# Optimization experiments

Hardware: AMD Instinct MI355X
Metric: run time of the kernel (lower is better)

## Reference

```python
import jax, jax.numpy as jnp
import numpy as np

N_EMBD = 768
N_HEAD = 8
HEAD_DIM = N_EMBD // N_HEAD
EPS = 1e-5


def _layernorm(x, g, b):
    mu = jnp.mean(x, axis=-1, keepdims=True)
    var = jnp.mean(jnp.square(x - mu), axis=-1, keepdims=True)
    return (x - mu) * jax.lax.rsqrt(var + EPS) * g + b


def _new_gelu(x):
    c = jnp.sqrt(2.0 / jnp.pi).astype(x.dtype)
    return 0.5 * x * (1.0 + jnp.tanh(c * (x + 0.044715 * x * x * x)))


def setup_inputs() -> dict:
    key = jax.random.key(0)
    ks = jax.random.split(key, 10)
    B, T, C = 16, 1024, N_EMBD
    s = lambda fan_in: 1.0 / np.sqrt(fan_in)
    inp = {
        "x": jax.random.normal(ks[0], (B, T, C), dtype=jnp.float32),
        "ln1_g": jnp.ones((C,), jnp.float32),
        "ln1_b": jnp.zeros((C,), jnp.float32),
        "attn_w": jax.random.normal(ks[1], (C, 3 * C), jnp.float32) * s(C),
        "attn_b": jnp.zeros((3 * C,), jnp.float32),
        "proj_w": jax.random.normal(ks[2], (C, C), jnp.float32) * s(C),
        "proj_b": jnp.zeros((C,), jnp.float32),
        "ln2_g": jnp.ones((C,), jnp.float32),
        "ln2_b": jnp.zeros((C,), jnp.float32),
        "fc_w": jax.random.normal(ks[3], (C, 4 * C), jnp.float32) * s(C),
        "fc_b": jnp.zeros((4 * C,), jnp.float32),
        "fc2_w": jax.random.normal(ks[4], (4 * C, C), jnp.float32) * s(4 * C),
        "fc2_b": jnp.zeros((C,), jnp.float32),
    }
    return inp


def reference(x, ln1_g, ln1_b, attn_w, attn_b, proj_w, proj_b,
              ln2_g, ln2_b, fc_w, fc_b, fc2_w, fc2_b):
    B, T, C = x.shape
    H, D = N_HEAD, HEAD_DIM
    scale = 1.0 / np.sqrt(D)

    # --- attention branch ---
    h = _layernorm(x, ln1_g, ln1_b)
    qkv = h @ attn_w + attn_b                       # [B,T,3C]
    q, k, v = jnp.split(qkv, 3, axis=-1)
    q = q.reshape(B, T, H, D).transpose(0, 2, 1, 3)  # [B,H,T,D]
    k = k.reshape(B, T, H, D).transpose(0, 2, 1, 3)
    v = v.reshape(B, T, H, D).transpose(0, 2, 1, 3)
    att = jnp.einsum("bhqd,bhkd->bhqk", q, k) * scale
    causal = jnp.tril(jnp.ones((T, T), bool))
    att = jnp.where(causal, att, -jnp.inf)
    att = jax.nn.softmax(att, axis=-1)
    y = jnp.einsum("bhqk,bhkd->bhqd", att, v)        # [B,H,T,D]
    y = y.transpose(0, 2, 1, 3).reshape(B, T, C)
    y = y @ proj_w + proj_b
    x = x + y

    # --- MLP branch ---
    h2 = _layernorm(x, ln2_g, ln2_b)
    h2 = _new_gelu(h2 @ fc_w + fc_b)
    x = x + (h2 @ fc2_w + fc2_b)
    return x
```

## Files before the change

kernel.cpp:

```cpp
#include <hip/hip_runtime.h>


typedef __bf16 bf16;
typedef __bf16 bf16x8 __attribute__((ext_vector_type(8)));
typedef __bf16 bf16x4 __attribute__((ext_vector_type(4)));
typedef __bf16 bf16x2 __attribute__((ext_vector_type(2)));
typedef float f32x4 __attribute__((ext_vector_type(4)));

__device__ __forceinline__ void async_copy16(const void* g, void* l)
{
    __builtin_amdgcn_global_load_lds((__attribute__((address_space(1))) void*)g,
                                     (__attribute__((address_space(3))) void*)l,
                                     16, 0, 0);
}

__device__ __forceinline__ void bar_nodrain()
{
    __builtin_amdgcn_sched_barrier(0);
    __asm__ volatile("" ::: "memory");
    __builtin_amdgcn_s_barrier();
    __asm__ volatile("" ::: "memory");
    __builtin_amdgcn_sched_barrier(0);
}

__global__ __launch_bounds__(256) void wtrans4(const float* __restrict__ aw, bf16* __restrict__ awT,
                                               const float* __restrict__ pw, bf16* __restrict__ pwT,
                                               const float* __restrict__ fw, bf16* __restrict__ fwT,
                                               const float* __restrict__ f2w, bf16* __restrict__ f2wT)
{
    __shared__ float tile[32][33];
    int id = blockIdx.x;
    const float* in; bf16* out; int R, C, nx;
    if (id < 1728)      { in = aw;  out = awT;  R = 768;  C = 2304; nx = 72; }
    else if (id < 2304) { in = pw;  out = pwT;  R = 768;  C = 768;  nx = 24; id -= 1728; }
    else if (id < 4608) { in = fw;  out = fwT;  R = 768;  C = 3072; nx = 96; id -= 2304; }
    else                { in = f2w; out = f2wT; R = 3072; C = 768;  nx = 24; id -= 4608; }
    const int c0 = (id % nx) * 32, r0 = (id / nx) * 32;
    const int tx = threadIdx.x, ty = threadIdx.y;
#pragma unroll
    for (int i = 0; i < 4; ++i)
        tile[ty + i * 8][tx] = in[(size_t)(r0 + ty + i * 8) * C + c0 + tx];
    __syncthreads();
#pragma unroll
    for (int i = 0; i < 4; ++i)
        out[(size_t)(c0 + ty + i * 8) * R + r0 + tx] = (bf16)tile[tx][ty + i * 8];
}

template <typename TIN>
__global__ __launch_bounds__(256) void ln_kernel(const TIN* __restrict__ x,
                                                 const float* __restrict__ g,
                                                 const float* __restrict__ bb,
                                                 bf16* __restrict__ out)
{
    const int wave = threadIdx.x >> 6, lane = threadIdx.x & 63;
    const size_t row = (size_t)blockIdx.x * 4 + wave;
    const TIN* xr = x + row * 768;
    float v[12];
    float s = 0.f;
#pragma unroll
    for (int c = 0; c < 3; ++c) {
        if constexpr (sizeof(TIN) == 2) {
            const bf16x4 t4 = *(const bf16x4*)(xr + c * 256 + lane * 4);
#pragma unroll
            for (int j = 0; j < 4; ++j) { v[c * 4 + j] = (float)t4[j]; s += v[c * 4 + j]; }
        } else {
            const float4 t4 = *(const float4*)(xr + c * 256 + lane * 4);
            v[c * 4 + 0] = t4.x; v[c * 4 + 1] = t4.y;
            v[c * 4 + 2] = t4.z; v[c * 4 + 3] = t4.w;
            s += t4.x + t4.y + t4.z + t4.w;
        }
    }
#pragma unroll
    for (int off = 32; off >= 1; off >>= 1) s += __shfl_xor(s, off, 64);
    const float mu = s * (1.f / 768.f);
    float q = 0.f;
#pragma unroll
    for (int i = 0; i < 12; ++i) { const float d = v[i] - mu; q += d * d; }
#pragma unroll
    for (int off = 32; off >= 1; off >>= 1) q += __shfl_xor(q, off, 64);
    const float rs = rsqrtf(q * (1.f / 768.f) + 1e-5f);
#pragma unroll
    for (int c = 0; c < 3; ++c) {
        const float4 gv = *(const float4*)(g + c * 256 + lane * 4);
        const float4 bv = *(const float4*)(bb + c * 256 + lane * 4);
        bf16x4 ov;
        ov[0] = (bf16)((v[c * 4 + 0] - mu) * rs * gv.x + bv.x);
        ov[1] = (bf16)((v[c * 4 + 1] - mu) * rs * gv.y + bv.y);
        ov[2] = (bf16)((v[c * 4 + 2] - mu) * rs * gv.z + bv.z);
        ov[3] = (bf16)((v[c * 4 + 3] - mu) * rs * gv.w + bv.w);
        *(bf16x4*)(out + row * 768 + c * 256 + lane * 4) = ov;
    }
}

template <int EPI, int TN>
__global__ __launch_bounds__(256) void gemm_bt(const bf16* __restrict__ A,
                                               const bf16* __restrict__ Bt,
                                               const float* __restrict__ bias,
                                               const void* __restrict__ res,
                                               void* __restrict__ out,
                                               const int M, const int N, const int K)
{
    constexpr int NT_W = TN / 32;
    constexpr int NCPB = (TN * 8) / 256;
    __shared__ bf16 sA[2 * 128 * 32];
    __shared__ bf16 sB[2 * TN * 32];
    const int t = threadIdx.x;
    const int wave = t >> 6, lane = t & 63;
    const int quad = lane >> 4, l16 = lane & 15;
    const int bm0 = blockIdx.x * 128, bn0 = blockIdx.y * TN;
    const int wm = (wave >> 1) * 64, wn = (wave & 1) * (TN / 2);

    const f32x4 z4 = {0.f, 0.f, 0.f, 0.f};
    f32x4 acc[4][NT_W];
#pragma unroll
    for (int i = 0; i < 4; ++i)
#pragma unroll
        for (int j = 0; j < NT_W; ++j) acc[i][j] = z4;

    const bf16* gAp[4]; bf16* lAp[4];
#pragma unroll
    for (int c = 0; c < 4; ++c) {
        const int j = c * 256 + t;
        const int img = j >> 9, r = (j >> 2) & 127, k8 = j & 3;
        gAp[c] = A + (size_t)(bm0 + r) * K + img * 32 + k8 * 8;
        lAp[c] = sA + j * 8;
    }
    const bf16* gBp[NCPB]; bf16* lBp[NCPB];
#pragma unroll
    for (int c = 0; c < NCPB; ++c) {
        const int j = c * 256 + t;
        const int img = j / (TN * 4), r = (j % (TN * 4)) >> 2, k8 = j & 3;
        gBp[c] = Bt + (size_t)(bn0 + r) * K + img * 32 + k8 * 8;
        lBp[c] = sB + j * 8;
    }

    for (int kt = 0; kt < K; kt += 64) {
        __syncthreads();
#pragma unroll
        for (int c = 0; c < 4; ++c) async_copy16(gAp[c] + kt, lAp[c]);
#pragma unroll
        for (int c = 0; c < NCPB; ++c) async_copy16(gBp[c] + kt, lBp[c]);
        __syncthreads();

#pragma unroll
        for (int ks = 0; ks < 2; ++ks) {
            bf16x8 af[4], bfm[NT_W];
#pragma unroll
            for (int mt = 0; mt < 4; ++mt)
                af[mt] = *(const bf16x8*)(sA + ks * 4096 +
                                          (wm + mt * 16 + l16) * 32 + quad * 8);
#pragma unroll
            for (int nt = 0; nt < NT_W; ++nt)
                bfm[nt] = *(const bf16x8*)(sB + ks * (TN * 32) +
                                           (wn + nt * 16 + l16) * 32 + quad * 8);
#pragma unroll
            for (int mt = 0; mt < 4; ++mt)
#pragma unroll
                for (int nt = 0; nt < NT_W; ++nt)
                    acc[mt][nt] = __builtin_amdgcn_mfma_f32_16x16x32_bf16(
                        af[mt], bfm[nt], acc[mt][nt], 0, 0, 0);
        }
    }

    const int rb = bm0 + wm + quad * 4;
    const int cb = bn0 + wn + l16;
#pragma unroll
    for (int mt = 0; mt < 4; ++mt) {
#pragma unroll
        for (int nt = 0; nt < NT_W; ++nt) {
            const int col = cb + nt * 16;
            const float bv = bias[col];
#pragma unroll
            for (int reg = 0; reg < 4; ++reg) {
                const size_t idx = (size_t)(rb + mt * 16 + reg) * N + col;
                float v = acc[mt][nt][reg] + bv;
                if constexpr (EPI == 1) {
                    ((bf16*)out)[idx] = (bf16)(v + ((const float*)res)[idx]);
                } else if constexpr (EPI == 2) {
                    const float u = v;
                    const float a2 = 1.5957691216057308f *
                                     (u + 0.044715f * u * u * u);
                    v = u / (1.f + __expf(-a2));
                    ((bf16*)out)[idx] = (bf16)v;
                } else if constexpr (EPI == 3) {
                    ((float*)out)[idx] = v + (float)((const bf16*)res)[idx];
                } else {
                    ((bf16*)out)[idx] = (bf16)v;
                }
            }
        }
    }
}

__global__ __launch_bounds__(256) void attn_kernel(const bf16* __restrict__ qkv,
                                                   bf16* __restrict__ aout)
{
    constexpr int T = 1024, C3 = 2304, HD = 96, CC = 768;
    __shared__ bf16 sK[64 * 104];
    __shared__ bf16 sV[96 * 72];
    __shared__ bf16 sP[4][16 * 76];
    const int tid = threadIdx.x;
    const int wave = tid >> 6, lane = tid & 63;
    const int quad = lane >> 4, l16 = lane & 15;
    const int bh = blockIdx.x, b = bh >> 3, h = bh & 7;
    const float scale = 0.10206207261596575f;

    const int qAi = blockIdx.y;
    const int qBi = 15 - qAi;
    const int q0A = qAi * 64 + wave * 16;
    const int q0B = qBi * 64 + wave * 16;

    const bf16* kgbase = qkv + (size_t)b * T * C3 + CC + h * HD;
    const bf16* vgbase = qkv + (size_t)b * T * C3 + 2 * CC + h * HD;
    bf16* sPw = &sP[wave][0];

    int kKey[3], kCh[3], vKey2[3], vDq[3];
#pragma unroll
    for (int c = 0; c < 3; ++c) {
        const int j = c * 256 + tid;
        kKey[c] = j / 12; kCh[c] = j - kKey[c] * 12;
        vKey2[c] = (j & 31) * 2; vDq[c] = j >> 5;
    }

    const bf16* qrA = qkv + (size_t)(b * T + q0A + l16) * C3 + h * HD + quad * 8;
    const bf16* qrB = qkv + (size_t)(b * T + q0B + l16) * C3 + h * HD + quad * 8;
    const bf16x8 aQA0 = *(const bf16x8*)(qrA);
    const bf16x8 aQA1 = *(const bf16x8*)(qrA + 32);
    const bf16x8 aQA2 = *(const bf16x8*)(qrA + 64);
    const bf16x8 aQB0 = *(const bf16x8*)(qrB);
    const bf16x8 aQB1 = *(const bf16x8*)(qrB + 32);
    const bf16x8 aQB2 = *(const bf16x8*)(qrB + 64);

    const f32x4 z4 = {0.f, 0.f, 0.f, 0.f};
    f32x4 oA[6], oB[6];
#pragma unroll
    for (int i = 0; i < 6; ++i) { oA[i] = z4; oB[i] = z4; }
    float lA[4] = {0.f, 0.f, 0.f, 0.f}, lB[4] = {0.f, 0.f, 0.f, 0.f};

    bf16x8 kreg[3];
    bf16x4 va[3], vb[3];
    auto issue_tile = [&](const int kk0) {
#pragma unroll
        for (int c = 0; c < 3; ++c) {
            kreg[c] = *(const bf16x8*)(kgbase + (size_t)(kk0 + kKey[c]) * C3 +
                                       kCh[c] * 8);
            const bf16* p0 = vgbase + (size_t)(kk0 + vKey2[c]) * C3 + vDq[c] * 4;
            va[c] = *(const bf16x4*)p0;
            vb[c] = *(const bf16x4*)(p0 + C3);
        }
    };

    auto process = [&](const bf16x8& Q0, const bf16x8& Q1, const bf16x8& Q2,
                       f32x4 (&o)[6], float (&lrow)[4],
                       const int q0, const int kk0, const bool diag) {
        f32x4 s[4];
#pragma unroll
        for (int i = 0; i < 4; ++i) s[i] = z4;
#pragma unroll
        for (int nt = 0; nt < 4; ++nt) {
            const bf16* kp = sK + (nt * 16 + l16) * 104 + quad * 8;
            const bf16x8 b0 = *(const bf16x8*)(kp);
            const bf16x8 b1 = *(const bf16x8*)(kp + 32);
            const bf16x8 b2 = *(const bf16x8*)(kp + 64);
            s[nt] = __builtin_amdgcn_mfma_f32_16x16x32_bf16(Q0, b0, s[nt], 0, 0, 0);
            s[nt] = __builtin_amdgcn_mfma_f32_16x16x32_bf16(Q1, b1, s[nt], 0, 0, 0);
            s[nt] = __builtin_amdgcn_mfma_f32_16x16x32_bf16(Q2, b2, s[nt], 0, 0, 0);
        }

        float psum[4] = {0.f, 0.f, 0.f, 0.f};
#pragma unroll
        for (int nt = 0; nt < 4; ++nt)
#pragma unroll
            for (int reg = 0; reg < 4; ++reg) {
                float v = s[nt][reg] * scale;
                if (diag) {
                    const int qr = q0 + quad * 4 + reg;
                    const int key = kk0 + nt * 16 + l16;
                    v = (key > qr) ? -1e30f : v;
                }
                const float p = __expf(fminf(v, 30.f));
                s[nt][reg] = p;
                psum[reg] += p;
            }

#pragma unroll
        for (int nt = 0; nt < 4; ++nt)
#pragma unroll
            for (int reg = 0; reg < 4; ++reg)
                sPw[(quad * 4 + reg) * 76 + nt * 16 + l16] = (bf16)s[nt][reg];
        __asm__ volatile("s_waitcnt lgkmcnt(0)" ::: "memory");

#pragma unroll
        for (int off = 1; off < 16; off <<= 1)
#pragma unroll
            for (int reg = 0; reg < 4; ++reg)
                psum[reg] += __shfl_xor(psum[reg], off, 64);
#pragma unroll
        for (int reg = 0; reg < 4; ++reg) lrow[reg] += psum[reg];

        const bf16x8 aP0 = *(const bf16x8*)(sPw + l16 * 76 + quad * 8);
        const bf16x8 aP1 = *(const bf16x8*)(sPw + l16 * 76 + 32 + quad * 8);
#pragma unroll
        for (int dd = 0; dd < 6; ++dd) {
            const bf16* vp = sV + (dd * 16 + l16) * 72 + quad * 8;
            const bf16x8 v0 = *(const bf16x8*)(vp);
            const bf16x8 v1 = *(const bf16x8*)(vp + 32);
            o[dd] = __builtin_amdgcn_mfma_f32_16x16x32_bf16(aP0, v0, o[dd], 0, 0, 0);
            o[dd] = __builtin_amdgcn_mfma_f32_16x16x32_bf16(aP1, v1, o[dd], 0, 0, 0);
        }
    };

    issue_tile(0);

    for (int kb = 0; kb <= qBi; ++kb) {
        const int kk0 = kb * 64;

        bar_nodrain();

#pragma unroll
        for (int c = 0; c < 3; ++c)
            *(bf16x8*)(sK + kKey[c] * 104 + kCh[c] * 8) = kreg[c];
#pragma unroll
        for (int c = 0; c < 3; ++c) {
#pragma unroll
            for (int jj = 0; jj < 4; ++jj) {
                bf16x2 pk; pk[0] = va[c][jj]; pk[1] = vb[c][jj];
                *(bf16x2*)(sV + (vDq[c] * 4 + jj) * 72 + vKey2[c]) = pk;
            }
        }

        if (kb < qBi) issue_tile(kk0 + 64);

        __asm__ volatile("s_waitcnt lgkmcnt(0)" ::: "memory");
        bar_nodrain();

        process(aQB0, aQB1, aQB2, oB, lB, q0B, kk0, kb == qBi);
        if (kb <= qAi)
            process(aQA0, aQA1, aQA2, oA, lA, q0A, kk0, kb == qAi);
    }

    bf16* opA = aout + (size_t)(b * T + q0A + quad * 4) * CC + h * HD + l16;
    bf16* opB = aout + (size_t)(b * T + q0B + quad * 4) * CC + h * HD + l16;
#pragma unroll
    for (int reg = 0; reg < 4; ++reg) {
        const float invA = 1.f / lA[reg];
        const float invB = 1.f / lB[reg];
#pragma unroll
        for (int dd = 0; dd < 6; ++dd) {
            opA[(size_t)reg * CC + dd * 16] = (bf16)(oA[dd][reg] * invA);
            opB[(size_t)reg * CC + dd * 16] = (bf16)(oB[dd][reg] * invB);
        }
    }
}

extern "C" void kernel_launch(void* const* d_in, const int* in_sizes, int n_in,
                              void* d_out, int out_size, void* d_ws, size_t ws_size,
                              hipStream_t stream)
{
    const float* x      = (const float*)d_in[0];
    const float* ln1_g  = (const float*)d_in[1];
    const float* ln1_b  = (const float*)d_in[2];
    const float* attn_w = (const float*)d_in[3];
    const float* attn_b = (const float*)d_in[4];
    const float* proj_w = (const float*)d_in[5];
    const float* proj_b = (const float*)d_in[6];
    const float* ln2_g  = (const float*)d_in[7];
    const float* ln2_b  = (const float*)d_in[8];
    const float* fc_w   = (const float*)d_in[9];
    const float* fc_b   = (const float*)d_in[10];
    const float* fc2_w  = (const float*)d_in[11];
    const float* fc2_b  = (const float*)d_in[12];

    char* ws = (char*)d_ws;
    bf16*  attn_wT = (bf16*)(ws + 0);
    bf16*  proj_wT = (bf16*)(ws + 3538944);
    bf16*  fc_wT   = (bf16*)(ws + 4718592);
    bf16*  fc2_wT  = (bf16*)(ws + 9437184);
    bf16*  hbuf    = (bf16*)(ws + 14155776);
    bf16*  qkv     = (bf16*)(ws + 39321600);
    bf16*  x1      = (bf16*)(ws + 39321600);
    bf16*  act     = (bf16*)(ws + 64487424);

    wtrans4<<<6912, dim3(32, 8), 0, stream>>>(attn_w, attn_wT, proj_w, proj_wT,
                                              fc_w, fc_wT, fc2_w, fc2_wT);

    ln_kernel<float><<<4096, 256, 0, stream>>>(x, ln1_g, ln1_b, hbuf);

    gemm_bt<0, 128><<<dim3(128, 18), 256, 0, stream>>>(
        hbuf, attn_wT, attn_b, nullptr, qkv, 16384, 2304, 768);

    attn_kernel<<<dim3(128, 8), 256, 0, stream>>>(qkv, hbuf);

    gemm_bt<1, 128><<<dim3(128, 6), 256, 0, stream>>>(
        hbuf, proj_wT, proj_b, x, x1, 16384, 768, 768);

    ln_kernel<bf16><<<4096, 256, 0, stream>>>(x1, ln2_g, ln2_b, hbuf);

    for (int c = 0; c < 2; ++c) {
        const size_t ro = (size_t)c * 8192;
        gemm_bt<2, 128><<<dim3(64, 24), 256, 0, stream>>>(
            hbuf + ro * 768, fc_wT, fc_b, nullptr, act, 8192, 3072, 768);
        gemm_bt<3, 64><<<dim3(64, 12), 256, 0, stream>>>(
            act, fc2_wT, fc2_b, x1 + ro * 768,
            (float*)d_out + ro * 768, 8192, 768, 3072);
    }
}
```

Baseline: 595.3 us.

## Double-buffer GEMM LDS tiles to overlap async loads with MFMA

The GEMM main loop used to load a 64-wide K slab into LDS and then compute on it, with a full barrier on each side. It now uses two 32-wide K buffers: the next slab is prefetched with async global-to-LDS copies while MFMAs run on the current one, followed by a vmcnt wait and a lightweight barrier. This aims to hide global memory latency behind compute. The cost is twice as many loop iterations and barriers for the same K range, since each step now covers only 32 of K.

New measurement: 609.7 us. 1.02x slower.

```diff
diff --git a/kernel.cpp b/kernel.cpp
--- a/kernel.cpp
+++ b/kernel.cpp
@@ -101,9 +101,10 @@
                                                const int M, const int N, const int K)
 {
     constexpr int NT_W = TN / 32;
-    constexpr int NCPB = (TN * 8) / 256;
-    __shared__ bf16 sA[2 * 128 * 32];
-    __shared__ bf16 sB[2 * TN * 32];
+    constexpr int NCPA = 2;
+    constexpr int NCPB = (TN * 4) / 256;
+    __shared__ bf16 sA[2][128 * 32];
+    __shared__ bf16 sB[2][TN * 32];
     const int t = threadIdx.x;
     const int wave = t >> 6, lane = t & 63;
     const int quad = lane >> 4, l16 = lane & 15;
@@ -117,49 +118,54 @@
 #pragma unroll
         for (int j = 0; j < NT_W; ++j) acc[i][j] = z4;
 
-    const bf16* gAp[4]; bf16* lAp[4];
-#pragma unroll
-    for (int c = 0; c < 4; ++c) {
+    const bf16* gAp[NCPA]; int lAo[NCPA];
+#pragma unroll
+    for (int c = 0; c < NCPA; ++c) {
         const int j = c * 256 + t;
-        const int img = j >> 9, r = (j >> 2) & 127, k8 = j & 3;
-        gAp[c] = A + (size_t)(bm0 + r) * K + img * 32 + k8 * 8;
-        lAp[c] = sA + j * 8;
-    }
-    const bf16* gBp[NCPB]; bf16* lBp[NCPB];
+        const int r = j >> 2, k8 = j & 3;
+        gAp[c] = A + (size_t)(bm0 + r) * K + k8 * 8;
+        lAo[c] = j * 8;
+    }
+    const bf16* gBp[NCPB]; int lBo[NCPB];
 #pragma unroll
     for (int c = 0; c < NCPB; ++c) {
         const int j = c * 256 + t;
-        const int img = j / (TN * 4), r = (j % (TN * 4)) >> 2, k8 = j & 3;
-        gBp[c] = Bt + (size_t)(bn0 + r) * K + img * 32 + k8 * 8;
-        lBp[c] = sB + j * 8;
-    }
-
-    for (int kt = 0; kt < K; kt += 64) {
-        __syncthreads();
-#pragma unroll
-        for (int c = 0; c < 4; ++c) async_copy16(gAp[c] + kt, lAp[c]);
-#pragma unroll
-        for (int c = 0; c < NCPB; ++c) async_copy16(gBp[c] + kt, lBp[c]);
-        __syncthreads();
-
-#pragma unroll
-        for (int ks = 0; ks < 2; ++ks) {
-            bf16x8 af[4], bfm[NT_W];
-#pragma unroll
-            for (int mt = 0; mt < 4; ++mt)
-                af[mt] = *(const bf16x8*)(sA + ks * 4096 +
-                                          (wm + mt * 16 + l16) * 32 + quad * 8);
+        const int r = j >> 2, k8 = j & 3;
+        gBp[c] = Bt + (size_t)(bn0 + r) * K + k8 * 8;
+        lBo[c] = j * 8;
+    }
+
+    auto stage = [&](const int buf, const int kt) {
+#pragma unroll
+        for (int c = 0; c < NCPA; ++c) async_copy16(gAp[c] + kt, &sA[buf][lAo[c]]);
+#pragma unroll
+        for (int c = 0; c < NCPB; ++c) async_copy16(gBp[c] + kt, &sB[buf][lBo[c]]);
+    };
+
+    stage(0, 0);
+    __syncthreads();
+
+    int cur = 0;
+    for (int kt = 0; kt < K; kt += 32) {
+        if (kt + 32 < K) stage(cur ^ 1, kt + 32);
+
+        bf16x8 af[4], bfm[NT_W];
+#pragma unroll
+        for (int mt = 0; mt < 4; ++mt)
+            af[mt] = *(const bf16x8*)(&sA[cur][(wm + mt * 16 + l16) * 32 + quad * 8]);
+#pragma unroll
+        for (int nt = 0; nt < NT_W; ++nt)
+            bfm[nt] = *(const bf16x8*)(&sB[cur][(wn + nt * 16 + l16) * 32 + quad * 8]);
+#pragma unroll
+        for (int mt = 0; mt < 4; ++mt)
 #pragma unroll
             for (int nt = 0; nt < NT_W; ++nt)
-                bfm[nt] = *(const bf16x8*)(sB + ks * (TN * 32) +
-                                           (wn + nt * 16 + l16) * 32 + quad * 8);
-#pragma unroll
-            for (int mt = 0; mt < 4; ++mt)
-#pragma unroll
-                for (int nt = 0; nt < NT_W; ++nt)
-                    acc[mt][nt] = __builtin_amdgcn_mfma_f32_16x16x32_bf16(
-                        af[mt], bfm[nt], acc[mt][nt], 0, 0, 0);
-        }
+                acc[mt][nt] = __builtin_amdgcn_mfma_f32_16x16x32_bf16(
+                    af[mt], bfm[nt], acc[mt][nt], 0, 0, 0);
+
+        __asm__ volatile("s_waitcnt vmcnt(0)" ::: "memory");
+        bar_nodrain();
+        cur ^= 1;
     }
 
     const int rb = bm0 + wm + quad * 4;
```
